# Performance work log

Hardware: AMD Instinct MI355X
Metric: run time of the kernel (lower is better)

## Reference

```python
import jax, jax.numpy as jnp
import numpy as np

TOP_N = 10
N_HEADS = 8

def _layernorm(x, g, b, eps=1e-5):
    mu = jnp.mean(x, axis=-1, keepdims=True)
    var = jnp.mean((x - mu) ** 2, axis=-1, keepdims=True)
    return (x - mu) * jax.lax.rsqrt(var + eps) * g + b

def setup_inputs() -> dict:
    key = jax.random.key(0)
    ks = jax.random.split(key, 16)
    B, N, D = 4096, 32768, 512
    s = 1.0 / np.sqrt(D)
    inp = {
        "visit_rep": jax.random.normal(ks[0], (B, D), jnp.float32),
        "E_mem_patient_rep": jax.random.normal(ks[1], (N, D), jnp.float32),
        "E_mem_med_rep": jax.random.normal(ks[2], (N, D), jnp.float32),
        "Wq": jax.random.uniform(ks[3], (D, D), jnp.float32, -s, s),
        "Wk": jax.random.uniform(ks[4], (D, D), jnp.float32, -s, s),
        "Wv": jax.random.uniform(ks[5], (D, D), jnp.float32, -s, s),
        "bq": jnp.zeros((D,), jnp.float32),
        "bk": jnp.zeros((D,), jnp.float32),
        "bv": jnp.zeros((D,), jnp.float32),
        "Wo": jax.random.uniform(ks[6], (D, D), jnp.float32, -s, s),
        "bo": jnp.zeros((D,), jnp.float32),
        "W1": jax.random.uniform(ks[7], (D, D), jnp.float32, -s, s),
        "b1": jax.random.uniform(ks[8], (D,), jnp.float32, -s, s),
        "W2": jax.random.uniform(ks[9], (D, D), jnp.float32, -s, s),
        "b2": jax.random.uniform(ks[10], (D,), jnp.float32, -s, s),
        "ln1_g": jnp.ones((D,), jnp.float32),
        "ln1_b": jnp.zeros((D,), jnp.float32),
        "ln2_g": jnp.ones((D,), jnp.float32),
        "ln2_b": jnp.zeros((D,), jnp.float32),
    }
    return inp

def reference(visit_rep, E_mem_patient_rep, E_mem_med_rep,
              Wq, bq, Wk, bk, Wv, bv, Wo, bo,
              W1, b1, W2, b2, ln1_g, ln1_b, ln2_g, ln2_b):
    B, D = visit_rep.shape
    H = N_HEADS
    hd = D // H
    # --- exact L2 kNN (faiss GpuIndexFlatL2 equivalent), detached ---
    q = jax.lax.stop_gradient(visit_rep)
    M = jax.lax.stop_gradient(E_mem_patient_rep)
    d2 = (jnp.sum(q * q, axis=1, keepdims=True)
          - 2.0 * q @ M.T
          + jnp.sum(M * M, axis=1)[None, :])          # [B, N]
    _, I = jax.lax.top_k(-d2, TOP_N)                    # [B, top_n]
    k = E_mem_patient_rep[I]                            # [B, top_n, D]
    v = E_mem_med_rep[I]                                # [B, top_n, D]
    # --- multihead attention, query seq-len 1 ---
    qh = (visit_rep @ Wq.T + bq).reshape(B, H, hd)
    kh = (k @ Wk.T + bk).reshape(B, TOP_N, H, hd)
    vh = (v @ Wv.T + bv).reshape(B, TOP_N, H, hd)
    scores = jnp.einsum("bhd,bnhd->bhn", qh, kh) / np.sqrt(hd)
    attn = jax.nn.softmax(scores, axis=-1)
    ctx = jnp.einsum("bhn,bnhd->bhd", attn, vh).reshape(B, D)
    attn_out = ctx @ Wo.T + bo
    # --- residual + norms + FFN (dropout = identity in eval) ---
    x = _layernorm(visit_rep + attn_out, ln1_g, ln1_b)
    ff = (jax.nn.leaky_relu(x @ W1.T + b1, 0.01)) @ W2.T + b2
    x = _layernorm(x + ff, ln2_g, ln2_b)
    return x
```

## Files before the change

### kernel.cpp

```cpp
#include <hip/hip_runtime.h>
#include <math.h>

#define BQ 4096
#define NMEM 32768
#define DD 512
#define TOPN 10
#define CB 256
#define ENT 2048
#define NCF 16
#define LK 6
#define SSTR 132
#define FINF 3.402823466e+38f
#define IMAX 0x7fffffff

typedef __attribute__((ext_vector_type(8))) short    bf16x8;
typedef __attribute__((ext_vector_type(4))) float    f32x4;

__device__ __forceinline__ unsigned short f2bf(float x) {
    unsigned int u = __float_as_uint(x);
    u += 0x7fffu + ((u >> 16) & 1u);
    return (unsigned short)(u >> 16);
}
__device__ __forceinline__ void async_copy16(const void* gp, void* lp) {
    __builtin_amdgcn_global_load_lds(
        (const __attribute__((address_space(1))) void*)gp,
        (__attribute__((address_space(3))) void*)lp, 16, 0, 0);
}
__device__ __forceinline__ bool lt_si(float s, int j, float s2, int j2) {
    return (s < s2) || (s == s2 && j < j2);
}
template<int KN>
__device__ __forceinline__ void topk_insert(float (&ts)[KN], int (&ti)[KN], float s, int j) {
    if (!lt_si(s, j, ts[KN-1], ti[KN-1])) return;
    #pragma unroll
    for (int p = KN-1; p > 0; --p) {
        if (lt_si(s, j, ts[p-1], ti[p-1])) { ts[p] = ts[p-1]; ti[p] = ti[p-1]; }
        else { ts[p] = s; ti[p] = j; return; }
    }
    ts[0] = s; ti[0] = j;
}

struct CastDesc {
    const float* in[7];
    unsigned short* out[7];
    int start[8];
};
__global__ __launch_bounds__(256) void cast_multi_kernel(CastDesc d) {
    int blk = blockIdx.x;
    int seg = 0;
    #pragma unroll
    for (int s = 0; s < 6; ++s) seg += (blk >= d.start[s + 1]) ? 1 : 0;
    int local = blk - d.start[seg];
    int i = (local * 256 + threadIdx.x) * 4;
    float4 v = *(const float4*)(d.in[seg] + i);
    ushort4 o;
    o.x = f2bf(v.x); o.y = f2bf(v.y); o.z = f2bf(v.z); o.w = f2bf(v.w);
    *(ushort4*)(d.out[seg] + i) = o;
}

__global__ __launch_bounds__(256) void cast_norm2_kernel(
        const float* __restrict__ inA, unsigned short* __restrict__ outA,
        const float* __restrict__ inB, unsigned short* __restrict__ outB,
        float* __restrict__ mnorm) {
    const float* in = blockIdx.y ? inB : inA;
    unsigned short* out = blockIdx.y ? outB : outA;
    int row = blockIdx.x * 4 + (threadIdx.x >> 6);
    int lane = threadIdx.x & 63;
    const float* r = in + (size_t)row * DD + lane * 8;
    float4 a = *(const float4*)r;
    float4 b = *(const float4*)(r + 4);
    ushort4 oa, ob;
    oa.x = f2bf(a.x); oa.y = f2bf(a.y); oa.z = f2bf(a.z); oa.w = f2bf(a.w);
    ob.x = f2bf(b.x); ob.y = f2bf(b.y); ob.z = f2bf(b.z); ob.w = f2bf(b.w);
    unsigned short* op = out + (size_t)row * DD + lane * 8;
    *(ushort4*)op = oa; *(ushort4*)(op + 4) = ob;
    if (blockIdx.y == 0) {
        float s = a.x*a.x + a.y*a.y + a.z*a.z + a.w*a.w
                + b.x*b.x + b.y*b.y + b.z*b.z + b.w*b.w;
        #pragma unroll
        for (int off = 32; off; off >>= 1) s += __shfl_xor(s, off, 64);
        if (lane == 0) mnorm[row] = s;
    }
}


__global__ __launch_bounds__(256) void gemm_knn_kernel(
        const unsigned short* __restrict__ Qb,
        const unsigned short* __restrict__ Mb,
        const float* __restrict__ mnorm,
        unsigned* __restrict__ cand_part) {
    __shared__ __align__(16) union {
        struct { unsigned short As[128 * 64]; unsigned short Bs[128 * 64]; } g;
        unsigned S[64 * SSTR];
    } sh;
    const int tid  = threadIdx.x;
    const int wave = tid >> 6, lane = tid & 63;
    const int quad = lane >> 4, c16 = lane & 15;
    const int m0 = blockIdx.y * 128, n0 = blockIdx.x * 128;
    const int wm0 = (wave >> 1) * 64, wn0 = (wave & 1) * 64;
    const int half = wave & 1;
    const int srow = wave * 32 + (lane >> 3);
    const int schunk = (lane & 7) ^ ((lane >> 3) & 7);
    const int xsw = c16 & 7;

    f32x4 acc[4][4] = {};

    for (int kt = 0; kt < DD; kt += 64) {
        __syncthreads();
        #pragma unroll
        for (int i = 0; i < 4; ++i) {
            const unsigned short* ga = Qb + (size_t)(m0 + srow + i * 8) * DD + kt + schunk * 8;
            async_copy16(ga, &sh.g.As[(wave * 32 + i * 8) * 64]);
            const unsigned short* gb = Mb + (size_t)(n0 + srow + i * 8) * DD + kt + schunk * 8;
            async_copy16(gb, &sh.g.Bs[(wave * 32 + i * 8) * 64]);
        }
        __syncthreads();
        #pragma unroll
        for (int ks = 0; ks < 64; ks += 32) {
            const int coff = (((ks >> 3) + quad) ^ xsw) << 3;
            bf16x8 af[4], bff[4];
            #pragma unroll
            for (int mt = 0; mt < 4; ++mt)
                af[mt] = *(const bf16x8*)&sh.g.As[(wm0 + mt * 16 + c16) * 64 + coff];
            #pragma unroll
            for (int nt = 0; nt < 4; ++nt)
                bff[nt] = *(const bf16x8*)&sh.g.Bs[(wn0 + nt * 16 + c16) * 64 + coff];
            #pragma unroll
            for (int mt = 0; mt < 4; ++mt)
                #pragma unroll
                for (int nt = 0; nt < 4; ++nt)
                    acc[mt][nt] = __builtin_amdgcn_mfma_f32_16x16x32_bf16(
                        af[mt], bff[nt], acc[mt][nt], 0, 0, 0);
        }
    }

    const int cbase = n0 + wn0 + c16;
    float mn[4];
    #pragma unroll
    for (int nt = 0; nt < 4; ++nt) mn[nt] = mnorm[cbase + nt * 16];

    const int rrow = tid >> 1, rhalf = tid & 1;
    unsigned q4[4] = {0xFFFFFFFFu, 0xFFFFFFFFu, 0xFFFFFFFFu, 0xFFFFFFFFu};

    __syncthreads();
    #pragma unroll
    for (int p = 0; p < 2; ++p) {
        #pragma unroll
        for (int mt = 0; mt < 4; ++mt)
            #pragma unroll
            for (int b = 0; b < 2; ++b) {
                const int nt = 2 * p + b;
                const int lcol = half * 64 + nt * 16 + c16;
                uint4 w;
                #pragma unroll
                for (int r = 0; r < 4; ++r) {
                    float s = fmaxf(fmaf(-2.f, acc[mt][nt][r], mn[nt]), 0.f);
                    (&w.x)[r] = (__float_as_uint(s) & 0xFFFFFF80u) | (unsigned)lcol;
                }
                const int slot = half * 32 + b * 16 + c16;
                *(uint4*)&sh.S[slot * SSTR + wm0 + mt * 16 + quad * 4] = w;
            }
        __syncthreads();
        #pragma unroll
        for (int m = 0; m < 32; ++m) {
            unsigned nv = sh.S[(rhalf * 32 + m) * SSTR + rrow];
            #pragma unroll
            for (int i = 0; i < 4; ++i) {
                unsigned lo = min(q4[i], nv);
                nv = max(q4[i], nv);
                q4[i] = lo;
            }
        }
        __syncthreads();
    }

    *(uint4*)(cand_part + (size_t)(m0 + rrow) * ENT + blockIdx.x * 8 + rhalf * 4) =
        make_uint4(q4[0], q4[1], q4[2], q4[3]);
}

__global__ __launch_bounds__(256) void knn_select_kernel(
        const unsigned* __restrict__ cand_part,
        const float* __restrict__ Q, const float* __restrict__ Mm,
        const float* __restrict__ mnorm,
        int* __restrict__ knn_idx) {
    const int row = blockIdx.x;
    const int wave = threadIdx.x >> 6, lane = threadIdx.x & 63;
    __shared__ unsigned sk[64];
    __shared__ int      sc[64];
    __shared__ int      ids[NCF];
    __shared__ float    d2s[NCF];

    unsigned ks[LK]; int ti[LK];
    #pragma unroll
    for (int q = 0; q < LK; ++q) { ks[q] = 0xFFFFFFFFu; ti[q] = IMAX; }
    const uint4* p4 = (const uint4*)(cand_part + (size_t)row * ENT) + wave * 128;
    #pragma unroll
    for (int i = 0; i < 2; ++i) {
        uint4 v = p4[lane + 64 * i];
        #pragma unroll
        for (int e = 0; e < 4; ++e) {
            unsigned k = (&v.x)[e];
            int pos = wave * 512 + (lane + 64 * i) * 4 + e;
            int gcol = (pos >> 3) * 128 + (int)(k & 127u);
            bool cm[LK];
            #pragma unroll
            for (int q = 0; q < LK; ++q) cm[q] = k < ks[q];
            #pragma unroll
            for (int q = LK - 1; q > 0; --q) {
                unsigned tns = cm[q] ? k : ks[q];  int tni = cm[q] ? gcol : ti[q];
                ks[q] = cm[q-1] ? ks[q-1] : tns;
                ti[q] = cm[q-1] ? ti[q-1] : tni;
            }
            ks[0] = cm[0] ? k : ks[0];
            ti[0] = cm[0] ? gcol : ti[0];
        }
    }
    #pragma unroll
    for (int r = 0; r < NCF; ++r) {
        unsigned mk = ks[0]; int mi = ti[0];
        #pragma unroll
        for (int off = 1; off < 64; off <<= 1) {
            unsigned ok = (unsigned)__shfl_xor((int)mk, off, 64);
            int      oi = __shfl_xor(mi, off, 64);
            bool t = (ok < mk) || (ok == mk && oi < mi);
            mk = t ? ok : mk; mi = t ? oi : mi;
        }
        bool win = (ks[0] == mk) && (ti[0] == mi);
        #pragma unroll
        for (int q = 0; q < LK - 1; ++q) {
            ks[q] = win ? ks[q+1] : ks[q];
            ti[q] = win ? ti[q+1] : ti[q];
        }
        ks[LK-1] = win ? 0xFFFFFFFFu : ks[LK-1];
        ti[LK-1] = win ? IMAX : ti[LK-1];
        if (lane == r) { sk[wave * NCF + r] = mk; sc[wave * NCF + r] = mi; }
    }
    __syncthreads();
    if (wave == 0) {
        unsigned myk = sk[lane];
        int      myc = sc[lane];
        #pragma unroll
        for (int r = 0; r < NCF; ++r) {
            unsigned mk = myk; int mi = myc;
            #pragma unroll
            for (int off = 1; off < 64; off <<= 1) {
                unsigned ok = (unsigned)__shfl_xor((int)mk, off, 64);
                int      oi = __shfl_xor(mi, off, 64);
                bool t = (ok < mk) || (ok == mk && oi < mi);
                mk = t ? ok : mk; mi = t ? oi : mi;
            }
            bool win = (myk == mk) && (myc == mi);
            myk = win ? 0xFFFFFFFFu : myk;
            myc = win ? IMAX : myc;
            if (lane == r) ids[r] = mi;
        }
    }
    __syncthreads();
    float4 q0 = *(const float4*)(Q + (size_t)row * DD + lane * 8);
    float4 q1 = *(const float4*)(Q + (size_t)row * DD + lane * 8 + 4);
    for (int c = wave; c < NCF; c += 4) {
        int j = ids[c];
        const float* mr = Mm + (size_t)j * DD;
        float4 m0 = *(const float4*)(mr + lane * 8);
        float4 m1 = *(const float4*)(mr + lane * 8 + 4);
        float dot = q0.x*m0.x + q0.y*m0.y + q0.z*m0.z + q0.w*m0.w
                  + q1.x*m1.x + q1.y*m1.y + q1.z*m1.z + q1.w*m1.w;
        #pragma unroll
        for (int off = 32; off; off >>= 1) dot += __shfl_xor(dot, off, 64);
        if (lane == 0) d2s[c] = fmaf(-2.f, dot, mnorm[j]);
    }
    __syncthreads();
    if (threadIdx.x == 0) {
        float ts[TOPN]; int tj[TOPN];
        #pragma unroll
        for (int p = 0; p < TOPN; ++p) { ts[p] = FINF; tj[p] = IMAX; }
        for (int c = 0; c < NCF; ++c) topk_insert<TOPN>(ts, tj, d2s[c], ids[c]);
        #pragma unroll
        for (int p = 0; p < TOPN; ++p) knn_idx[row * TOPN + p] = tj[p];
    }
}

template<int ACT, int OUT_BF16>
__global__ __launch_bounds__(256) void gemm_bf16_nt(
        const unsigned short* __restrict__ A,
        const unsigned short* __restrict__ B,
        const float* __restrict__ bias,
        void* __restrict__ Cout, int ldc) {
    __shared__ __align__(16) unsigned short As[128 * 64];
    __shared__ __align__(16) unsigned short Bs[128 * 64];
    const int tid  = threadIdx.x;
    const int wave = tid >> 6, lane = tid & 63;
    const int quad = lane >> 4, c16 = lane & 15;
    const int m0 = blockIdx.y * 128, n0 = blockIdx.x * 128;
    const int wm0 = (wave >> 1) * 64, wn0 = (wave & 1) * 64;
    const int srow = wave * 32 + (lane >> 3);
    const int schunk = (lane & 7) ^ ((lane >> 3) & 7);
    const int xsw = c16 & 7;

    f32x4 acc[4][4] = {};

    for (int kt = 0; kt < DD; kt += 64) {
        __syncthreads();
        #pragma unroll
        for (int i = 0; i < 4; ++i) {
            const unsigned short* ga = A + (size_t)(m0 + srow + i * 8) * DD + kt + schunk * 8;
            async_copy16(ga, &As[(wave * 32 + i * 8) * 64]);
            const unsigned short* gb = B + (size_t)(n0 + srow + i * 8) * DD + kt + schunk * 8;
            async_copy16(gb, &Bs[(wave * 32 + i * 8) * 64]);
        }
        __syncthreads();
        #pragma unroll
        for (int ks = 0; ks < 64; ks += 32) {
            const int coff = (((ks >> 3) + quad) ^ xsw) << 3;
            bf16x8 af[4], bff[4];
            #pragma unroll
            for (int mt = 0; mt < 4; ++mt)
                af[mt] = *(const bf16x8*)&As[(wm0 + mt * 16 + c16) * 64 + coff];
            #pragma unroll
            for (int nt = 0; nt < 4; ++nt)
                bff[nt] = *(const bf16x8*)&Bs[(wn0 + nt * 16 + c16) * 64 + coff];
            #pragma unroll
            for (int mt = 0; mt < 4; ++mt)
                #pragma unroll
                for (int nt = 0; nt < 4; ++nt)
                    acc[mt][nt] = __builtin_amdgcn_mfma_f32_16x16x32_bf16(
                        af[mt], bff[nt], acc[mt][nt], 0, 0, 0);
        }
    }
    #pragma unroll
    for (int nt = 0; nt < 4; ++nt) {
        int ncol = n0 + wn0 + nt * 16 + c16;
        float bv = bias[ncol];
        #pragma unroll
        for (int mt = 0; mt < 4; ++mt) {
            size_t rbase = (size_t)(m0 + wm0 + mt * 16 + quad * 4) * ldc + ncol;
            #pragma unroll
            for (int r = 0; r < 4; ++r) {
                float v = acc[mt][nt][r] + bv;
                if (ACT == 1) v = v >= 0.f ? v : 0.01f * v;
                if (OUT_BF16) ((unsigned short*)Cout)[rbase + (size_t)r * ldc] = f2bf(v);
                else          ((float*)Cout)[rbase + (size_t)r * ldc] = v;
            }
        }
    }
}

struct G3 {
    const unsigned short* A[3];
    const unsigned short* B[3];
    const float* bias[3];
    void* C[3];
    int obf[3];
};
__global__ __launch_bounds__(256) void gemm3_kernel(G3 g) {
    const int yy = blockIdx.y;
    const int z = (yy >= 512) ? 2 : (yy >= 256 ? 1 : 0);
    const int my = yy - z * 256;
    __shared__ __align__(16) unsigned short As[128 * 64];
    __shared__ __align__(16) unsigned short Bs[128 * 64];
    const unsigned short* A = g.A[z];
    const unsigned short* B = g.B[z];
    const int tid  = threadIdx.x;
    const int wave = tid >> 6, lane = tid & 63;
    const int quad = lane >> 4, c16 = lane & 15;
    const int m0 = my * 128, n0 = blockIdx.x * 128;
    const int wm0 = (wave >> 1) * 64, wn0 = (wave & 1) * 64;
    const int srow = wave * 32 + (lane >> 3);
    const int schunk = (lane & 7) ^ ((lane >> 3) & 7);
    const int xsw = c16 & 7;

    f32x4 acc[4][4] = {};

    for (int kt = 0; kt < DD; kt += 64) {
        __syncthreads();
        #pragma unroll
        for (int i = 0; i < 4; ++i) {
            const unsigned short* ga = A + (size_t)(m0 + srow + i * 8) * DD + kt + schunk * 8;
            async_copy16(ga, &As[(wave * 32 + i * 8) * 64]);
            const unsigned short* gb = B + (size_t)(n0 + srow + i * 8) * DD + kt + schunk * 8;
            async_copy16(gb, &Bs[(wave * 32 + i * 8) * 64]);
        }
        __syncthreads();
        #pragma unroll
        for (int ks = 0; ks < 64; ks += 32) {
            const int coff = (((ks >> 3) + quad) ^ xsw) << 3;
            bf16x8 af[4], bff[4];
            #pragma unroll
            for (int mt = 0; mt < 4; ++mt)
                af[mt] = *(const bf16x8*)&As[(wm0 + mt * 16 + c16) * 64 + coff];
            #pragma unroll
            for (int nt = 0; nt < 4; ++nt)
                bff[nt] = *(const bf16x8*)&Bs[(wn0 + nt * 16 + c16) * 64 + coff];
            #pragma unroll
            for (int mt = 0; mt < 4; ++mt)
                #pragma unroll
                for (int nt = 0; nt < 4; ++nt)
                    acc[mt][nt] = __builtin_amdgcn_mfma_f32_16x16x32_bf16(
                        af[mt], bff[nt], acc[mt][nt], 0, 0, 0);
        }
    }
    const int obf = g.obf[z];
    #pragma unroll
    for (int nt = 0; nt < 4; ++nt) {
        int ncol = n0 + wn0 + nt * 16 + c16;
        float bv = g.bias[z][ncol];
        #pragma unroll
        for (int mt = 0; mt < 4; ++mt) {
            size_t rbase = (size_t)(m0 + wm0 + mt * 16 + quad * 4) * DD + ncol;
            #pragma unroll
            for (int r = 0; r < 4; ++r) {
                float v = acc[mt][nt][r] + bv;
                if (obf) ((unsigned short*)g.C[z])[rbase + (size_t)r * DD] = f2bf(v);
                else     ((float*)g.C[z])[rbase + (size_t)r * DD] = v;
            }
        }
    }
}

__global__ __launch_bounds__(512) void attn_kernel(
        const float* __restrict__ qh, const unsigned short* __restrict__ Kall,
        const unsigned short* __restrict__ Vall, const int* __restrict__ knn_idx,
        unsigned short* __restrict__ ctx_b) {
    const int b = blockIdx.x;
    const int h = threadIdx.x >> 6;
    const int l = threadIdx.x & 63;
    const int col = (h << 6) + l;
    int idxs[TOPN];
    #pragma unroll
    for (int n = 0; n < TOPN; ++n) idxs[n] = knn_idx[b * TOPN + n];
    const float q = qh[(size_t)b * DD + col];
    float sc[TOPN];
    #pragma unroll
    for (int n = 0; n < TOPN; ++n) {
        float p = q * __uint_as_float((unsigned)Kall[(size_t)idxs[n] * DD + col] << 16);
        #pragma unroll
        for (int off = 32; off; off >>= 1) p += __shfl_xor(p, off, 64);
        sc[n] = p * 0.125f;
    }
    float mx = sc[0];
    #pragma unroll
    for (int n = 1; n < TOPN; ++n) mx = fmaxf(mx, sc[n]);
    float se = 0.f;
    #pragma unroll
    for (int n = 0; n < TOPN; ++n) { sc[n] = expf(sc[n] - mx); se += sc[n]; }
    const float inv = 1.f / se;
    float o = 0.f;
    #pragma unroll
    for (int n = 0; n < TOPN; ++n)
        o = fmaf(sc[n] * inv,
                 __uint_as_float((unsigned)Vall[(size_t)idxs[n] * DD + col] << 16), o);
    ctx_b[(size_t)b * DD + col] = f2bf(o);
}

template<int EMIT_BF16>
__global__ __launch_bounds__(256) void add_ln_kernel(
        const float* __restrict__ X, const float* __restrict__ Y,
        const float* __restrict__ g, const float* __restrict__ be,
        float* __restrict__ out, unsigned short* __restrict__ out_b) {
    const int row = blockIdx.x;
    const int t = threadIdx.x;
    const size_t base = (size_t)row * DD;
    float v0 = X[base + t]       + Y[base + t];
    float v1 = X[base + 256 + t] + Y[base + 256 + t];
    float s = v0 + v1, sq = v0 * v0 + v1 * v1;
    #pragma unroll
    for (int off = 32; off; off >>= 1) { s += __shfl_xor(s, off, 64); sq += __shfl_xor(sq, off, 64); }
    __shared__ float rs[4], rq[4];
    const int w = t >> 6, l = t & 63;
    if (l == 0) { rs[w] = s; rq[w] = sq; }
    __syncthreads();
    float tot  = rs[0] + rs[1] + rs[2] + rs[3];
    float totq = rq[0] + rq[1] + rq[2] + rq[3];
    float mu = tot * (1.f / DD);
    float var = totq * (1.f / DD) - mu * mu;
    float rstd = rsqrtf(var + 1e-5f);
    float o0 = (v0 - mu) * rstd * g[t]       + be[t];
    float o1 = (v1 - mu) * rstd * g[256 + t] + be[256 + t];
    out[base + t] = o0;
    out[base + 256 + t] = o1;
    if (EMIT_BF16) {
        out_b[base + t] = f2bf(o0);
        out_b[base + 256 + t] = f2bf(o1);
    }
}

extern "C" void kernel_launch(void* const* d_in, const int* in_sizes, int n_in,
                              void* d_out, int out_size, void* d_ws, size_t ws_size,
                              hipStream_t stream) {
    const float* visit = (const float*)d_in[0];
    const float* Epat  = (const float*)d_in[1];
    const float* Emed  = (const float*)d_in[2];
    const float* Wq = (const float*)d_in[3];
    const float* Wk = (const float*)d_in[4];
    const float* Wv = (const float*)d_in[5];
    const float* bq = (const float*)d_in[6];
    const float* bk = (const float*)d_in[7];
    const float* bv = (const float*)d_in[8];
    const float* Wo = (const float*)d_in[9];
    const float* bo = (const float*)d_in[10];
    const float* W1 = (const float*)d_in[11];
    const float* b1 = (const float*)d_in[12];
    const float* W2 = (const float*)d_in[13];
    const float* b2 = (const float*)d_in[14];
    const float* ln1g = (const float*)d_in[15];
    const float* ln1b = (const float*)d_in[16];
    const float* ln2g = (const float*)d_in[17];
    const float* ln2b = (const float*)d_in[18];
    float* out = (float*)d_out;

    char* base = (char*)d_ws;
    const size_t MB = 1u << 20;
    float* mnorm   = (float*)(base);
    int*   knn_idx = (int*)  (base + 2*MB);
    float* qh      = (float*)(base + 3*MB);
    float* attn_o  = qh;
    float* x1      = (float*)(base + 11*MB);
    float* ff      = (float*)(base + 19*MB);
    unsigned short* Qb    = (unsigned short*)(base + 27*MB);
    unsigned short* ctx_b = (unsigned short*)(base + 31*MB);
    unsigned short* x1_b  = (unsigned short*)(base + 35*MB);
    unsigned short* h1_b  = (unsigned short*)(base + 39*MB);
    unsigned short* Wq_b  = (unsigned short*)(base + 43*MB);
    unsigned short* Wk_b  = Wq_b + 262144;
    unsigned short* Wv_b  = Wk_b + 262144;
    unsigned short* Wo_b  = Wv_b + 262144;
    unsigned short* W1_b  = Wo_b + 262144;
    unsigned short* W2_b  = W1_b + 262144;
    unsigned short* Mb     = (unsigned short*)(base + 46*MB);
    unsigned short* Emed_b = (unsigned short*)(base + 78*MB);
    unsigned short* Kall = (unsigned short*)(base + 110*MB);
    unsigned short* Vall = Kall + (size_t)NMEM * DD;
    unsigned* cand_part = (unsigned*)Kall;

    cast_norm2_kernel<<<dim3(NMEM / 4, 2), 256, 0, stream>>>(Epat, Mb, Emed, Emed_b, mnorm);
    CastDesc cd;
    cd.in[0] = visit; cd.out[0] = Qb;
    cd.in[1] = Wq; cd.in[2] = Wk; cd.in[3] = Wv; cd.in[4] = Wo; cd.in[5] = W1; cd.in[6] = W2;
    cd.out[1] = Wq_b; cd.out[2] = Wk_b; cd.out[3] = Wv_b; cd.out[4] = Wo_b; cd.out[5] = W1_b; cd.out[6] = W2_b;
    cd.start[0] = 0; cd.start[1] = 2048;
    for (int s = 2; s <= 7; ++s) cd.start[s] = cd.start[s-1] + 256;
    cast_multi_kernel<<<cd.start[7], 256, 0, stream>>>(cd);

    gemm_knn_kernel<<<dim3(CB, BQ / 128), 256, 0, stream>>>(Qb, Mb, mnorm, cand_part);
    knn_select_kernel<<<BQ, 256, 0, stream>>>(cand_part, visit, Epat, mnorm, knn_idx);

    G3 g3;
    g3.A[0] = Mb;     g3.B[0] = Wk_b; g3.bias[0] = bk; g3.C[0] = Kall; g3.obf[0] = 1;
    g3.A[1] = Emed_b; g3.B[1] = Wv_b; g3.bias[1] = bv; g3.C[1] = Vall; g3.obf[1] = 1;
    g3.A[2] = Qb;     g3.B[2] = Wq_b; g3.bias[2] = bq; g3.C[2] = qh;   g3.obf[2] = 0;
    gemm3_kernel<<<dim3(4, 544), 256, 0, stream>>>(g3);

    attn_kernel<<<BQ, 512, 0, stream>>>(qh, Kall, Vall, knn_idx, ctx_b);

    gemm_bf16_nt<0,0><<<dim3(4, BQ / 128), 256, 0, stream>>>(ctx_b, Wo_b, bo, attn_o, DD);
    add_ln_kernel<1><<<BQ, 256, 0, stream>>>(visit, attn_o, ln1g, ln1b, x1, x1_b);
    gemm_bf16_nt<1,1><<<dim3(4, BQ / 128), 256, 0, stream>>>(x1_b, W1_b, b1, h1_b, DD);
    gemm_bf16_nt<0,0><<<dim3(4, BQ / 128), 256, 0, stream>>>(h1_b, W2_b, b2, ff,   DD);
    add_ln_kernel<0><<<BQ, 256, 0, stream>>>(x1, ff, ln2g, ln2b, out, nullptr);
}
```

Baseline: 599.4 us.

## Enlarge kNN GEMM tile to 256x256 with 4-stage async LDS pipeline

```diff
diff --git a/kernel.cpp b/kernel.cpp
--- a/kernel.cpp
+++ b/kernel.cpp
@@ -5,11 +5,10 @@
 #define NMEM 32768
 #define DD 512
 #define TOPN 10
-#define CB 256
+#define NBX 128
 #define ENT 2048
 #define NCF 16
 #define LK 6
-#define SSTR 132
 #define FINF 3.402823466e+38f
 #define IMAX 0x7fffffff
 
@@ -83,87 +82,109 @@
     }
 }
 
-
-__global__ __launch_bounds__(256) void gemm_knn_kernel(
+__global__ __launch_bounds__(512, 2) void gemm_knn_kernel(
         const unsigned short* __restrict__ Qb,
         const unsigned short* __restrict__ Mb,
         const float* __restrict__ mnorm,
         unsigned* __restrict__ cand_part) {
     __shared__ __align__(16) union {
-        struct { unsigned short As[128 * 64]; unsigned short Bs[128 * 64]; } g;
-        unsigned S[64 * SSTR];
+        struct { unsigned short A[4][256][32]; unsigned short B[4][256][32]; } g;
+        unsigned S[64 * 260];
     } sh;
     const int tid  = threadIdx.x;
-    const int wave = tid >> 6, lane = tid & 63;
+    const int lane = tid & 63;
+    const int wave = tid >> 6;
     const int quad = lane >> 4, c16 = lane & 15;
-    const int m0 = blockIdx.y * 128, n0 = blockIdx.x * 128;
-    const int wm0 = (wave >> 1) * 64, wn0 = (wave & 1) * 64;
-    const int half = wave & 1;
-    const int srow = wave * 32 + (lane >> 3);
-    const int schunk = (lane & 7) ^ ((lane >> 3) & 7);
-    const int xsw = c16 & 7;
-
-    f32x4 acc[4][4] = {};
-
-    for (int kt = 0; kt < DD; kt += 64) {
+    const int wm = wave >> 2, wn = wave & 3;
+    const int m0 = blockIdx.y * 256, n0 = blockIdx.x * 256;
+    const int srow   = tid >> 2;
+    const int schunk = (tid & 3) ^ (srow & 3);
+    const unsigned short* ag = Qb + (size_t)(m0 + srow) * DD + schunk * 8;
+    const unsigned short* bg = Mb + (size_t)(n0 + srow) * DD + schunk * 8;
+    const int cq = (quad ^ (c16 & 3)) * 8;
+
+    f32x4  acc[8][4] = {};
+    bf16x8 af[2][8], bf[2][4];
+
+#define KSTAGE(tt) do {                                                         \
+    const int s_ = (tt) & 3;                                                    \
+    async_copy16(ag + (tt)*32,           &sh.g.A[s_][srow][(tid & 3) * 8]);     \
+    async_copy16(ag + (tt)*32 + 128*DD,  &sh.g.A[s_][128 + srow][(tid & 3) * 8]);\
+    async_copy16(bg + (tt)*32,           &sh.g.B[s_][srow][(tid & 3) * 8]);     \
+    async_copy16(bg + (tt)*32 + 128*DD,  &sh.g.B[s_][128 + srow][(tid & 3) * 8]);\
+} while (0)
+
+#define KREAD(tt, st) do {                                                      \
+    const int s_ = (tt) & 3;                                                    \
+    _Pragma("unroll")                                                           \
+    for (int mt = 0; mt < 8; ++mt)                                              \
+        af[st][mt] = *(const bf16x8*)&sh.g.A[s_][wm*128 + mt*16 + c16][cq];     \
+    _Pragma("unroll")                                                           \
+    for (int nt = 0; nt < 4; ++nt)                                              \
+        bf[st][nt] = *(const bf16x8*)&sh.g.B[s_][wn*64 + nt*16 + c16][cq];      \
+} while (0)
+
+#define KMFMA(st) do {                                                          \
+    _Pragma("unroll")                                                           \
+    for (int mt = 0; mt < 8; ++mt)                                              \
+        _Pragma("unroll")                                                       \
+        for (int nt = 0; nt < 4; ++nt)                                          \
+            acc[mt][nt] = __builtin_amdgcn_mfma_f32_16x16x32_bf16(              \
+                af[st][mt], bf[st][nt], acc[mt][nt], 0, 0, 0);                  \
+} while (0)
+
+    KSTAGE(0); KSTAGE(1); KSTAGE(2);
+    asm volatile("s_waitcnt vmcnt(8)" ::: "memory");
+    __builtin_amdgcn_s_barrier();
+    __builtin_amdgcn_sched_barrier(0);
+    KREAD(0, 0);
+
+    #pragma unroll
+    for (int t = 0; t < 16; ++t) {
+        if (t < 14)       asm volatile("s_waitcnt vmcnt(4)" ::: "memory");
+        else if (t == 14) asm volatile("s_waitcnt vmcnt(0)" ::: "memory");
+        if (t < 15) {
+            __builtin_amdgcn_s_barrier();
+            __builtin_amdgcn_sched_barrier(0);
+            KREAD(t + 1, (t + 1) & 1);
+        }
+        if (t + 3 < 16) KSTAGE(t + 3);
+        __builtin_amdgcn_sched_barrier(0);
+        __builtin_amdgcn_s_setprio(1);
+        KMFMA(t & 1);
+        __builtin_amdgcn_s_setprio(0);
+    }
+#undef KSTAGE
+#undef KREAD
+#undef KMFMA
+
+    float mn[4];
+    #pragma unroll
+    for (int nt = 0; nt < 4; ++nt) mn[nt] = mnorm[n0 + wn*64 + nt*16 + c16];
+    const int rrow = tid >> 1, rhalf = tid & 1;
+    __syncthreads();
+    #pragma unroll
+    for (int p = 0; p < 4; ++p) {
+        if (wn == p) {
+            #pragma unroll
+            for (int mt = 0; mt < 8; ++mt)
+                #pragma unroll
+                for (int nt = 0; nt < 4; ++nt) {
+                    uint4 w;
+                    #pragma unroll
+                    for (int r = 0; r < 4; ++r) {
+                        float s = fmaxf(fmaf(-2.f, acc[mt][nt][r], mn[nt]), 0.f);
+                        (&w.x)[r] = (__float_as_uint(s) & 0xFFFFFF80u)
+                                  | (unsigned)((p & 1) * 64 + nt * 16 + c16);
+                    }
+                    *(uint4*)&sh.S[(nt*16 + c16) * 260 + wm*128 + mt*16 + quad*4] = w;
+                }
+        }
         __syncthreads();
-        #pragma unroll
-        for (int i = 0; i < 4; ++i) {
-            const unsigned short* ga = Qb + (size_t)(m0 + srow + i * 8) * DD + kt + schunk * 8;
-            async_copy16(ga, &sh.g.As[(wave * 32 + i * 8) * 64]);
-            const unsigned short* gb = Mb + (size_t)(n0 + srow + i * 8) * DD + kt + schunk * 8;
-            async_copy16(gb, &sh.g.Bs[(wave * 32 + i * 8) * 64]);
-        }
-        __syncthreads();
-        #pragma unroll
-        for (int ks = 0; ks < 64; ks += 32) {
-            const int coff = (((ks >> 3) + quad) ^ xsw) << 3;
-            bf16x8 af[4], bff[4];
-            #pragma unroll
-            for (int mt = 0; mt < 4; ++mt)
-                af[mt] = *(const bf16x8*)&sh.g.As[(wm0 + mt * 16 + c16) * 64 + coff];
-            #pragma unroll
-            for (int nt = 0; nt < 4; ++nt)
-                bff[nt] = *(const bf16x8*)&sh.g.Bs[(wn0 + nt * 16 + c16) * 64 + coff];
-            #pragma unroll
-            for (int mt = 0; mt < 4; ++mt)
-                #pragma unroll
-                for (int nt = 0; nt < 4; ++nt)
-                    acc[mt][nt] = __builtin_amdgcn_mfma_f32_16x16x32_bf16(
-                        af[mt], bff[nt], acc[mt][nt], 0, 0, 0);
-        }
-    }
-
-    const int cbase = n0 + wn0 + c16;
-    float mn[4];
-    #pragma unroll
-    for (int nt = 0; nt < 4; ++nt) mn[nt] = mnorm[cbase + nt * 16];
-
-    const int rrow = tid >> 1, rhalf = tid & 1;
-    unsigned q4[4] = {0xFFFFFFFFu, 0xFFFFFFFFu, 0xFFFFFFFFu, 0xFFFFFFFFu};
-
-    __syncthreads();
-    #pragma unroll
-    for (int p = 0; p < 2; ++p) {
-        #pragma unroll
-        for (int mt = 0; mt < 4; ++mt)
-            #pragma unroll
-            for (int b = 0; b < 2; ++b) {
-                const int nt = 2 * p + b;
-                const int lcol = half * 64 + nt * 16 + c16;
-                uint4 w;
-                #pragma unroll
-                for (int r = 0; r < 4; ++r) {
-                    float s = fmaxf(fmaf(-2.f, acc[mt][nt][r], mn[nt]), 0.f);
-                    (&w.x)[r] = (__float_as_uint(s) & 0xFFFFFF80u) | (unsigned)lcol;
-                }
-                const int slot = half * 32 + b * 16 + c16;
-                *(uint4*)&sh.S[slot * SSTR + wm0 + mt * 16 + quad * 4] = w;
-            }
-        __syncthreads();
+        unsigned q4[4] = {0xFFFFFFFFu, 0xFFFFFFFFu, 0xFFFFFFFFu, 0xFFFFFFFFu};
         #pragma unroll
         for (int m = 0; m < 32; ++m) {
-            unsigned nv = sh.S[(rhalf * 32 + m) * SSTR + rrow];
+            unsigned nv = sh.S[(rhalf*32 + m) * 260 + rrow];
             #pragma unroll
             for (int i = 0; i < 4; ++i) {
                 unsigned lo = min(q4[i], nv);
@@ -171,11 +192,18 @@
                 q4[i] = lo;
             }
         }
+        unsigned p0 = (unsigned)__shfl_xor((int)q4[0], 1, 64);
+        unsigned p1 = (unsigned)__shfl_xor((int)q4[1], 1, 64);
+        unsigned p2 = (unsigned)__shfl_xor((int)q4[2], 1, 64);
+        unsigned p3 = (unsigned)__shfl_xor((int)q4[3], 1, 64);
+        if (rhalf == 0) {
+            uint4 w4;
+            w4.x = min(q4[0], p3); w4.y = min(q4[1], p2);
+            w4.z = min(q4[2], p1); w4.w = min(q4[3], p0);
+            *(uint4*)(cand_part + (size_t)(m0 + rrow) * ENT + blockIdx.x * 16 + p * 4) = w4;
+        }
         __syncthreads();
     }
-
-    *(uint4*)(cand_part + (size_t)(m0 + rrow) * ENT + blockIdx.x * 8 + rhalf * 4) =
-        make_uint4(q4[0], q4[1], q4[2], q4[3]);
 }
 
 __global__ __launch_bounds__(256) void knn_select_kernel(
@@ -541,7 +569,7 @@
     for (int s = 2; s <= 7; ++s) cd.start[s] = cd.start[s-1] + 256;
     cast_multi_kernel<<<cd.start[7], 256, 0, stream>>>(cd);
 
-    gemm_knn_kernel<<<dim3(CB, BQ / 128), 256, 0, stream>>>(Qb, Mb, mnorm, cand_part);
+    gemm_knn_kernel<<<dim3(NBX, BQ / 256), 512, 0, stream>>>(Qb, Mb, mnorm, cand_part);
     knn_select_kernel<<<BQ, 256, 0, stream>>>(cand_part, visit, Epat, mnorm, knn_idx);
 
     G3 g3;
```

Result: no change. 603.2 us (+0.6%).
